# Optimization experiments

Measured on AMD Instinct MI355X. Metric: run time of the kernel, lower is better.

The kernel has to match this reference:

```python
import jax, jax.numpy as jnp
import numpy as np

D_MODEL = 1024
NUM_HEADS = 16
D_HEAD = D_MODEL // NUM_HEADS
POS_VOCAB = 512
ROPE_BASE = 10000.0


def _rope_sin_cos(seq_len, d_head, dtype=jnp.float32):
    inv_freq = 1.0 / (ROPE_BASE ** (jnp.arange(0, d_head, 2, dtype=jnp.float32) / d_head))
    pos = jnp.arange(seq_len, dtype=jnp.float32)
    freqs = pos[:, None] * inv_freq[None, :]            # [S, d_head/2]
    sin = jnp.repeat(jnp.sin(freqs), 2, axis=-1)        # [S, d_head] (repeat_interleave)
    cos = jnp.repeat(jnp.cos(freqs), 2, axis=-1)
    return sin.astype(dtype), cos.astype(dtype)


def _rotate_half(x):
    # interleaved pairs: (x0,x1,x2,x3,...) -> (-x1,x0,-x3,x2,...)
    x1 = x[..., ::2]
    x2 = x[..., 1::2]
    return jnp.stack((-x2, x1), axis=-1).reshape(x.shape)


def setup_inputs() -> dict:
    key = jax.random.key(0)
    ks = jax.random.split(key, 12)
    B, S = 2, 2048
    sc = 1.0 / np.sqrt(D_MODEL)
    inp = {
        "x": jax.random.normal(ks[0], (B, S, D_MODEL), jnp.float32),
        "dist_matrix": jax.random.randint(ks[1], (B, S, S), 0, POS_VOCAB, jnp.int32),
        "Wq": jax.random.normal(ks[2], (D_MODEL, D_MODEL), jnp.float32) * sc,
        "bq": jnp.zeros((D_MODEL,), jnp.float32),
        "Wk": jax.random.normal(ks[3], (D_MODEL, D_MODEL), jnp.float32) * sc,
        "bk": jnp.zeros((D_MODEL,), jnp.float32),
        "Wv": jax.random.normal(ks[4], (D_MODEL, D_MODEL), jnp.float32) * sc,
        "bv": jnp.zeros((D_MODEL,), jnp.float32),
        "Wo": jax.random.normal(ks[5], (D_MODEL, D_MODEL), jnp.float32) * sc,
        "bo": jnp.zeros((D_MODEL,), jnp.float32),
        "bias_table": jax.random.normal(ks[6], (POS_VOCAB, NUM_HEADS), jnp.float32) * 0.02,
    }
    return inp


def reference(x, dist_matrix, Wq, bq, Wk, bk, Wv, bv, Wo, bo, bias_table):
    B, S, _ = x.shape
    H, Dh = NUM_HEADS, D_HEAD

    def proj(W, b):
        return (x @ W + b).reshape(B, S, H, Dh).transpose(0, 2, 1, 3)  # [B,H,S,Dh]

    Q = proj(Wq, bq)
    K = proj(Wk, bk)
    V = proj(Wv, bv)

    sin, cos = _rope_sin_cos(S, Dh, x.dtype)  # [S, Dh]
    Q = Q * cos + _rotate_half(Q) * sin
    K = K * cos + _rotate_half(K) * sin

    scores = jnp.einsum("bhqd,bhkd->bhqk", Q, K) / jnp.sqrt(jnp.asarray(Dh, x.dtype))

    pad_mask = dist_matrix < 0                                 # [B,S,S]
    idx = jnp.clip(dist_matrix, 0, None)
    rel_bias = bias_table[idx]                                 # [B,S,S,H]
    rel_bias = jnp.where(pad_mask[..., None], 0.0, rel_bias)
    scores = scores + rel_bias.transpose(0, 3, 1, 2)           # [B,H,S,S]

    attn = jax.nn.softmax(scores, axis=-1)
    out = jnp.einsum("bhqk,bhkd->bhqd", attn, V)
    out = out.transpose(0, 2, 1, 3).reshape(B, S, H * Dh)
    return out @ Wo + bo
```

## Files before the change

### kernel.cpp

```cpp
#include <hip/hip_runtime.h>
#include <hip/hip_bf16.h>
#include <math.h>

#define B_   2
#define S_   2048
#define H_   16
#define DH_  64
#define DM_  1024
#define M_   (B_*S_)
#define PV_  512
#define LOG2E 1.4426950408889634f

typedef __attribute__((ext_vector_type(8))) short bf16x8;
typedef __attribute__((ext_vector_type(4))) float f32x4;

__device__ __forceinline__ float b2f(unsigned short u) {
  union { unsigned int i; float f; } v; v.i = ((unsigned int)u) << 16; return v.f;
}
__device__ __forceinline__ unsigned short f2b(float f) {
  union { float f; unsigned int i; } v; v.f = f;
  return (unsigned short)((v.i + 0x7fffu + ((v.i >> 16) & 1u)) >> 16);
}
__device__ __forceinline__ f32x4 mfma16(bf16x8 a, bf16x8 b, f32x4 c) {
  return __builtin_amdgcn_mfma_f32_16x16x32_bf16(a, b, c, 0, 0, 0);
}
__device__ __forceinline__ unsigned int cvtpk(float a, float b) {
  unsigned int r;
  asm("v_cvt_pk_bf16_f32 %0, %1, %2" : "=v"(r) : "v"(a), "v"(b));
  return r;
}

__global__ void k_ropetab(float* tab) {
  int idx = blockIdx.x * 256 + threadIdx.x;
  if (idx >= S_ * 32) return;
  int s = idx >> 5, i = idx & 31;
  double inv = exp(-((double)(2 * i) / 64.0) * log(10000.0));
  double f = (double)s * inv;
  tab[idx * 2 + 0] = (float)sin(f);
  tab[idx * 2 + 1] = (float)cos(f);
}

__global__ __launch_bounds__(256) void k_prep(const float* __restrict__ x,
                                              const float* __restrict__ Wq,
                                              const float* __restrict__ Wk,
                                              const float* __restrict__ Wv,
                                              const float* __restrict__ Wo,
                                              float* __restrict__ tab,
                                              unsigned short* __restrict__ Wtall,
                                              unsigned short* __restrict__ xb) {
  __shared__ unsigned short t[64][65];
  int bid = blockIdx.x;
  if (bid < 256) {
    int idx = bid * 256 + threadIdx.x;
    int s = idx >> 5, i = idx & 31;
    double inv = exp(-((double)(2 * i) / 64.0) * log(10000.0));
    double f = (double)s * inv;
    tab[idx * 2 + 0] = (float)sin(f);
    tab[idx * 2 + 1] = (float)cos(f);
  } else if (bid < 1280) {
    int tw = bid - 256;
    int wid = tw >> 8, sub = tw & 255;
    const float* W = (wid == 0) ? Wq : (wid == 1) ? Wk : (wid == 2) ? Wv : Wo;
    unsigned short* Wt = Wtall + (size_t)wid * DM_ * DM_;
    int r0 = (sub >> 4) * 64, c0 = (sub & 15) * 64;
    #pragma unroll
    for (int p = 0; p < 16; ++p) {
      int idx = p * 256 + threadIdx.x;
      int i = idx >> 6, j = idx & 63;
      t[i][j] = f2b(W[(size_t)(r0 + i) * DM_ + c0 + j]);
    }
    __syncthreads();
    #pragma unroll
    for (int p = 0; p < 16; ++p) {
      int idx = p * 256 + threadIdx.x;
      int i = idx >> 6, j = idx & 63;
      Wt[(size_t)(c0 + i) * DM_ + r0 + j] = t[j][i];
    }
  } else {
    int idx = (bid - 1280) * 256 + threadIdx.x;
    const float4 f0 = *(const float4*)(x + (size_t)idx * 8);
    const float4 f1 = *(const float4*)(x + (size_t)idx * 8 + 4);
    union { uint4 u; unsigned short s[8]; } o;
    o.s[0] = f2b(f0.x); o.s[1] = f2b(f0.y); o.s[2] = f2b(f0.z); o.s[3] = f2b(f0.w);
    o.s[4] = f2b(f1.x); o.s[5] = f2b(f1.y); o.s[6] = f2b(f1.z); o.s[7] = f2b(f1.w);
    *(uint4*)(xb + (size_t)idx * 8) = o.u;
  }
}

__global__ __launch_bounds__(256) void k_gemmQKV(const unsigned short* __restrict__ A,
                                                 const unsigned short* __restrict__ Wtall,
                                                 const float* __restrict__ bq,
                                                 const float* __restrict__ bk,
                                                 const float* __restrict__ bv,
                                                 unsigned short* __restrict__ Qr,
                                                 unsigned short* __restrict__ Kr,
                                                 unsigned short* __restrict__ Vp,
                                                 const float* __restrict__ tab,
                                                 float qscale) {
  __shared__ unsigned short Alds[128][40];
  __shared__ unsigned short Blds[128][40];
  int lane = threadIdx.x & 63, w = threadIdx.x >> 6;
  int wr = w >> 1, wc = w & 1;
  int l16 = lane & 15, lq = lane >> 4;
  int m0 = blockIdx.y * 128, n0 = blockIdx.x * 128;
  f32x4 acc[4][4];
  #pragma unroll
  for (int a = 0; a < 4; ++a)
    #pragma unroll
    for (int b = 0; b < 4; ++b) acc[a][b] = (f32x4){0.f, 0.f, 0.f, 0.f};

  for (int k0 = 0; k0 < DM_; k0 += 32) {
    __syncthreads();
    #pragma unroll
    for (int i = 0; i < 2; ++i) {
      int c = threadIdx.x + i * 256;
      int r = c >> 2, ch = (c & 3) * 8;
      *(uint4*)&Alds[r][ch] = *(const uint4*)(A + (size_t)(m0 + r) * DM_ + k0 + ch);
      *(uint4*)&Blds[r][ch] = *(const uint4*)(Wtall + (size_t)(n0 + r) * DM_ + k0 + ch);
    }
    __syncthreads();
    bf16x8 af[4], bf_[4];
    #pragma unroll
    for (int mi = 0; mi < 4; ++mi) af[mi] = *(const bf16x8*)&Alds[wr * 64 + mi * 16 + l16][lq * 8];
    #pragma unroll
    for (int ni = 0; ni < 4; ++ni) bf_[ni] = *(const bf16x8*)&Blds[wc * 64 + ni * 16 + l16][lq * 8];
    #pragma unroll
    for (int mi = 0; mi < 4; ++mi)
      #pragma unroll
      for (int ni = 0; ni < 4; ++ni)
        acc[mi][ni] = mfma16(af[mi], bf_[ni], acc[mi][ni]);
  }

  int proj = n0 >> 10;
  const float* bs = (proj == 0) ? bq : (proj == 1) ? bk : bv;
  float scale = (proj == 0) ? qscale : 1.0f;
  unsigned short* R = (proj == 0) ? Qr : Kr;
  #pragma unroll
  for (int ni = 0; ni < 4; ++ni) {
    int col = n0 + wc * 64 + ni * 16 + l16;
    int c = col & 1023;
    float bvv = bs[c];
    if (proj < 2) {
      int h = c >> 6, d = c & 63;
      #pragma unroll
      for (int mi = 0; mi < 4; ++mi)
        #pragma unroll
        for (int j = 0; j < 4; ++j) {
          int row = m0 + wr * 64 + mi * 16 + lq * 4 + j;
          int s = row & (S_ - 1), b = row >> 11;
          float v = acc[mi][ni][j] + bvv;
          float p = __shfl_xor(v, 1, 64);
          float2 sc = *(const float2*)(tab + ((size_t)s * 32 + (d >> 1)) * 2);
          float o = (d & 1) ? (v * sc.y + p * sc.x)
                            : (v * sc.y - p * sc.x);
          R[(((size_t)(b * H_ + h) * S_) + s) * DH_ + d] = f2b(o * scale);
        }
    } else {
      #pragma unroll
      for (int mi = 0; mi < 4; ++mi)
        #pragma unroll
        for (int j = 0; j < 4; ++j) {
          int row = m0 + wr * 64 + mi * 16 + lq * 4 + j;
          Vp[(size_t)row * DM_ + c] = f2b(acc[mi][ni][j] + bvv);
        }
    }
  }
}

template<bool AF32, bool ROPE, bool OF32, bool WB16>
__global__ __launch_bounds__(256) void k_gemmW(const void* __restrict__ Av,
                                               const void* __restrict__ Wv,
                                               const float* __restrict__ bias,
                                               void* __restrict__ Cv,
                                               const float* __restrict__ tab,
                                               int M, int N, int K, float scale) {
  __shared__ unsigned short Alds[128][40];
  __shared__ unsigned short Blds[128][40];
  int lane = threadIdx.x & 63, w = threadIdx.x >> 6;
  int wr = w >> 1, wc = w & 1;
  int l16 = lane & 15, lq = lane >> 4;
  int m0 = blockIdx.y * 128, n0 = blockIdx.x * 128;
  f32x4 acc[4][4];
  #pragma unroll
  for (int a = 0; a < 4; ++a)
    #pragma unroll
    for (int b = 0; b < 4; ++b) acc[a][b] = (f32x4){0.f, 0.f, 0.f, 0.f};

  for (int k0 = 0; k0 < K; k0 += 32) {
    __syncthreads();
    #pragma unroll
    for (int i = 0; i < 2; ++i) {
      int c = threadIdx.x + i * 256;
      int r = c >> 2, ch = (c & 3) * 8;
      size_t base = (size_t)(m0 + r) * K + k0 + ch;
      if (AF32) {
        const float* A = (const float*)Av;
        float4 f0 = *(const float4*)(A + base);
        float4 f1 = *(const float4*)(A + base + 4);
        unsigned short* dst = &Alds[r][ch];
        dst[0] = f2b(f0.x); dst[1] = f2b(f0.y); dst[2] = f2b(f0.z); dst[3] = f2b(f0.w);
        dst[4] = f2b(f1.x); dst[5] = f2b(f1.y); dst[6] = f2b(f1.z); dst[7] = f2b(f1.w);
      } else {
        *(uint4*)&Alds[r][ch] = *(const uint4*)((const unsigned short*)Av + base);
      }
    }
    if (WB16) {
      #pragma unroll
      for (int i = 0; i < 2; ++i) {
        int c = threadIdx.x + i * 256;
        int r = c >> 2, ch = (c & 3) * 8;
        *(uint4*)&Blds[r][ch] =
            *(const uint4*)((const unsigned short*)Wv + (size_t)(n0 + r) * K + k0 + ch);
      }
    } else {
      #pragma unroll
      for (int i = 0; i < 2; ++i) {
        int c = threadIdx.x + i * 256;
        int kk = c >> 4, n8 = (c & 15) * 8;
        size_t base = (size_t)(k0 + kk) * N + n0 + n8;
        const float* W = (const float*)Wv;
        float4 w0 = *(const float4*)(W + base);
        float4 w1 = *(const float4*)(W + base + 4);
        Blds[n8 + 0][kk] = f2b(w0.x); Blds[n8 + 1][kk] = f2b(w0.y);
        Blds[n8 + 2][kk] = f2b(w0.z); Blds[n8 + 3][kk] = f2b(w0.w);
        Blds[n8 + 4][kk] = f2b(w1.x); Blds[n8 + 5][kk] = f2b(w1.y);
        Blds[n8 + 6][kk] = f2b(w1.z); Blds[n8 + 7][kk] = f2b(w1.w);
      }
    }
    __syncthreads();
    bf16x8 af[4], bf_[4];
    #pragma unroll
    for (int mi = 0; mi < 4; ++mi) af[mi] = *(const bf16x8*)&Alds[wr * 64 + mi * 16 + l16][lq * 8];
    #pragma unroll
    for (int ni = 0; ni < 4; ++ni) bf_[ni] = *(const bf16x8*)&Blds[wc * 64 + ni * 16 + l16][lq * 8];
    #pragma unroll
    for (int mi = 0; mi < 4; ++mi)
      #pragma unroll
      for (int ni = 0; ni < 4; ++ni)
        acc[mi][ni] = mfma16(af[mi], bf_[ni], acc[mi][ni]);
  }
  if (!ROPE) {
    #pragma unroll
    for (int ni = 0; ni < 4; ++ni) {
      int col = n0 + wc * 64 + ni * 16 + l16;
      float bv = bias[col];
      #pragma unroll
      for (int mi = 0; mi < 4; ++mi)
        #pragma unroll
        for (int j = 0; j < 4; ++j) {
          int row = m0 + wr * 64 + mi * 16 + lq * 4 + j;
          size_t idx = (size_t)row * N + col;
          float v = acc[mi][ni][j] + bv;
          if (OF32) ((float*)Cv)[idx] = v;
          else      ((unsigned short*)Cv)[idx] = f2b(v);
        }
    }
  } else {
    #pragma unroll
    for (int ni = 0; ni < 4; ++ni) {
      int col = n0 + wc * 64 + ni * 16 + l16;
      int h = col >> 6, d = col & 63;
      float bv = bias[col];
      #pragma unroll
      for (int mi = 0; mi < 4; ++mi)
        #pragma unroll
        for (int j = 0; j < 4; ++j) {
          int row = m0 + wr * 64 + mi * 16 + lq * 4 + j;
          int s = row & (S_ - 1), b = row >> 11;
          float v = acc[mi][ni][j] + bv;
          float p = __shfl_xor(v, 1, 64);
          float2 sc = *(const float2*)(tab + ((size_t)s * 32 + (d >> 1)) * 2);
          float o = (d & 1) ? (v * sc.y + p * sc.x)
                            : (v * sc.y - p * sc.x);
          ((unsigned short*)Cv)[(((size_t)(b * H_ + h) * S_) + s) * DH_ + d] = f2b(o * scale);
        }
    }
  }
}

__global__ __launch_bounds__(256) void k_vtrans(const unsigned short* __restrict__ Vp,
                                                unsigned short* __restrict__ Vt) {
  int bid = blockIdx.x;
  int st = bid & 31; int bh = bid >> 5; int h = bh & 15; int b = bh >> 4;
  int s0 = st * 64;
  __shared__ unsigned short t[64][72];
  #pragma unroll
  for (int i = 0; i < 2; ++i) {
    int c = threadIdx.x + i * 256;
    int r = c >> 3, ch = (c & 7) * 8;
    *(uint4*)&t[r][ch] = *(const uint4*)(Vp + (size_t)(b * S_ + s0 + r) * DM_ + h * DH_ + ch);
  }
  __syncthreads();
  #pragma unroll
  for (int i = 0; i < 2; ++i) {
    int c = threadIdx.x + i * 256;
    int dr = c >> 3, ch = (c & 7) * 8;
    union { uint4 u; unsigned short x[8]; } tb;
    #pragma unroll
    for (int e = 0; e < 8; ++e) tb.x[e] = t[ch + e][dr];
    *(uint4*)(Vt + ((size_t)bh * DH_ + dr) * S_ + s0 + ch) = tb.u;
  }
}

__global__ __launch_bounds__(512) void k_attn(const unsigned short* __restrict__ Qr,
                                              const unsigned short* __restrict__ Kr,
                                              const unsigned short* __restrict__ Vt,
                                              const int* __restrict__ dist,
                                              const float* __restrict__ table,
                                              unsigned short* __restrict__ AO) {
  int bid = blockIdx.x;
  int qt = bid & 15; int bh = bid >> 4; int h = bh & 15; int b = bh >> 4;
  int lane = threadIdx.x & 63, w = threadIdx.x >> 6;
  int l16 = lane & 15, lq = lane >> 4;
  int q0 = qt * 128;

  __shared__ unsigned short Klds[64][72];
  __shared__ unsigned short Vlds[64][72];
  __shared__ unsigned short Plds[8][16][72];
  __shared__ float tlds[PV_];

  for (int i = threadIdx.x; i < PV_; i += 512) tlds[i] = table[i * H_ + h] * LOG2E;

  const unsigned short* Qbase = Qr + ((size_t)bh * S_ + q0 + w * 16 + l16) * DH_;
  bf16x8 aq0 = *(const bf16x8*)(Qbase + lq * 8);
  bf16x8 aq1 = *(const bf16x8*)(Qbase + 32 + lq * 8);

  f32x4 oacc[4];
  float m_[4], l_[4];
  #pragma unroll
  for (int j = 0; j < 4; ++j) { m_[j] = -1e30f; l_[j] = 0.f; }
  #pragma unroll
  for (int td = 0; td < 4; ++td) oacc[td] = (f32x4){0.f, 0.f, 0.f, 0.f};

  const int* drow = dist + ((size_t)b * S_ + q0 + w * 16) * S_;
  const unsigned short* Ksrc0 = Kr + (size_t)bh * S_ * DH_;
  const unsigned short* Vsrc0 = Vt + (size_t)bh * DH_ * S_;

  int dc[4][4], dn[4][4];
  #pragma unroll
  for (int j = 0; j < 4; ++j) {
    const int* dr = drow + (size_t)(lq * 4 + j) * S_;
    #pragma unroll
    for (int t = 0; t < 4; ++t) dc[j][t] = dr[t * 16 + l16];
  }

  for (int kv = 0; kv < S_; kv += 64) {
    __syncthreads();
    {
      const unsigned short* Ksrc = Ksrc0 + (size_t)kv * DH_;
      const unsigned short* Vsrc = Vsrc0 + kv;
      int c = threadIdx.x;
      int r = c >> 3, ch = (c & 7) * 8;
      *(uint4*)&Klds[r][ch] = *(const uint4*)(Ksrc + (size_t)r * DH_ + ch);
      *(uint4*)&Vlds[r][ch] = *(const uint4*)(Vsrc + (size_t)r * S_ + ch);
    }
    {
      int kvn = (kv + 64 < S_) ? kv + 64 : 0;
      #pragma unroll
      for (int j = 0; j < 4; ++j) {
        const int* dr = drow + (size_t)(lq * 4 + j) * S_ + kvn;
        #pragma unroll
        for (int t = 0; t < 4; ++t) dn[j][t] = dr[t * 16 + l16];
      }
    }
    __syncthreads();

    f32x4 sc[4];
    #pragma unroll
    for (int t = 0; t < 4; ++t) {
      bf16x8 bk0 = *(const bf16x8*)&Klds[t * 16 + l16][lq * 8];
      bf16x8 bk1 = *(const bf16x8*)&Klds[t * 16 + l16][32 + lq * 8];
      f32x4 z = (f32x4){0.f, 0.f, 0.f, 0.f};
      z = mfma16(aq0, bk0, z);
      z = mfma16(aq1, bk1, z);
      sc[t] = z;
    }

    float rm[4];
    #pragma unroll
    for (int j = 0; j < 4; ++j) {
      float best = -1e30f;
      #pragma unroll
      for (int t = 0; t < 4; ++t) {
        float s = sc[t][j] + tlds[dc[j][t]];
        sc[t][j] = s;
        best = fmaxf(best, s);
      }
      rm[j] = best;
    }

    bool need = (rm[0] > m_[0] + 11.5416f) || (rm[1] > m_[1] + 11.5416f) ||
                (rm[2] > m_[2] + 11.5416f) || (rm[3] > m_[3] + 11.5416f);
    if (__any(need)) {
      #pragma unroll
      for (int off = 1; off < 16; off <<= 1) {
        #pragma unroll
        for (int j = 0; j < 4; ++j) rm[j] = fmaxf(rm[j], __shfl_xor(rm[j], off, 64));
      }
      #pragma unroll
      for (int j = 0; j < 4; ++j) {
        float mn = fmaxf(m_[j], rm[j]);
        float scl = exp2f(m_[j] - mn);
        l_[j] *= scl;
        #pragma unroll
        for (int td = 0; td < 4; ++td) oacc[td][j] *= scl;
        m_[j] = mn;
      }
    }

    float p[4][4];
    #pragma unroll
    for (int j = 0; j < 4; ++j) {
      float su = 0.f;
      #pragma unroll
      for (int t = 0; t < 4; ++t) {
        float e = exp2f(sc[t][j] - m_[j]);
        p[t][j] = e;
        su += e;
      }
      l_[j] += su;
    }

    #pragma unroll
    for (int j = 0; j < 4; ++j) {
      unsigned int r01 = cvtpk(p[0][j], p[1][j]);
      unsigned int r23 = cvtpk(p[2][j], p[3][j]);
      Plds[w][lq * 4 + j][l16]      = (unsigned short)r01;
      Plds[w][lq * 4 + j][16 + l16] = (unsigned short)(r01 >> 16);
      Plds[w][lq * 4 + j][32 + l16] = (unsigned short)r23;
      Plds[w][lq * 4 + j][48 + l16] = (unsigned short)(r23 >> 16);
    }

    bf16x8 pa0 = *(const bf16x8*)&Plds[w][l16][lq * 8];
    bf16x8 pa1 = *(const bf16x8*)&Plds[w][l16][32 + lq * 8];
    #pragma unroll
    for (int td = 0; td < 4; ++td) {
      bf16x8 v0 = *(const bf16x8*)&Vlds[td * 16 + l16][lq * 8];
      bf16x8 v1 = *(const bf16x8*)&Vlds[td * 16 + l16][32 + lq * 8];
      oacc[td] = mfma16(pa0, v0, oacc[td]);
      oacc[td] = mfma16(pa1, v1, oacc[td]);
    }

    #pragma unroll
    for (int j = 0; j < 4; ++j)
      #pragma unroll
      for (int t = 0; t < 4; ++t) dc[j][t] = dn[j][t];
  }

  #pragma unroll
  for (int off = 1; off < 16; off <<= 1) {
    #pragma unroll
    for (int j = 0; j < 4; ++j) l_[j] += __shfl_xor(l_[j], off, 64);
  }
  float inv[4];
  #pragma unroll
  for (int j = 0; j < 4; ++j) inv[j] = 1.f / l_[j];
  #pragma unroll
  for (int td = 0; td < 4; ++td) {
    #pragma unroll
    for (int j = 0; j < 4; ++j) {
      size_t row = (size_t)b * S_ + q0 + w * 16 + lq * 4 + j;
      AO[row * DM_ + h * DH_ + td * 16 + l16] = f2b(oacc[td][j] * inv[j]);
    }
  }
}

extern "C" void kernel_launch(void* const* d_in, const int* in_sizes, int n_in,
                              void* d_out, int out_size, void* d_ws, size_t ws_size,
                              hipStream_t stream) {
  const float* x    = (const float*)d_in[0];
  const int*   dist = (const int*)d_in[1];
  const float* Wq   = (const float*)d_in[2];
  const float* bq   = (const float*)d_in[3];
  const float* Wk   = (const float*)d_in[4];
  const float* bk   = (const float*)d_in[5];
  const float* Wv   = (const float*)d_in[6];
  const float* bv   = (const float*)d_in[7];
  const float* Wo   = (const float*)d_in[8];
  const float* bo   = (const float*)d_in[9];
  const float* tabb = (const float*)d_in[10];

  char* ws = (char*)d_ws;
  const size_t SZ_TAB = (size_t)S_ * 32 * 2 * 4;
  const size_t SZ_T   = (size_t)M_ * DM_ * 2;
  const size_t SZ_W   = (size_t)DM_ * DM_ * 2;
  float* rtab = (float*)ws;
  size_t off = SZ_TAB;
  unsigned short* Qr   = (unsigned short*)(ws + off); off += SZ_T;
  unsigned short* Kr   = (unsigned short*)(ws + off); off += SZ_T;
  unsigned short* Vt   = (unsigned short*)(ws + off); off += SZ_T;
  unsigned short* VpAO = (unsigned short*)(ws + off); off += SZ_T;
  unsigned short* Wtall = (unsigned short*)(ws + off); off += 4 * SZ_W;
  size_t off_prep = off;
  unsigned short* xb   = (unsigned short*)(ws + off); off += SZ_T;
  bool prep  = ws_size >= off_prep;
  bool xcast = ws_size >= off;

  const float QSCALE = 0.125f * LOG2E;

  if (prep && xcast) {
    k_prep<<<dim3(3328), 256, 0, stream>>>(x, Wq, Wk, Wv, Wo, rtab, Wtall, xb);
    k_gemmQKV<<<dim3(24, 32), 256, 0, stream>>>(xb, Wtall, bq, bk, bv, Qr, Kr, VpAO, rtab, QSCALE);
  } else {
    k_ropetab<<<dim3(256), dim3(256), 0, stream>>>(rtab);
    k_gemmW<true, true,  false, false><<<dim3(8, 32), 256, 0, stream>>>(x, Wq, bq, Qr, rtab, M_, DM_, DM_, QSCALE);
    k_gemmW<true, true,  false, false><<<dim3(8, 32), 256, 0, stream>>>(x, Wk, bk, Kr, rtab, M_, DM_, DM_, 1.0f);
    k_gemmW<true, false, false, false><<<dim3(8, 32), 256, 0, stream>>>(x, Wv, bv, VpAO, rtab, M_, DM_, DM_, 1.0f);
  }
  k_vtrans<<<dim3(1024), 256, 0, stream>>>(VpAO, Vt);

  k_attn<<<dim3(512), dim3(512), 0, stream>>>(Qr, Kr, Vt, dist, tabb, VpAO);

  if (prep && xcast) {
    k_gemmW<false, false, true, true><<<dim3(8, 32), 256, 0, stream>>>(
        VpAO, Wtall + (size_t)3 * DM_ * DM_, bo, d_out, rtab, M_, DM_, DM_, 1.0f);
  } else {
    k_gemmW<false, false, true, false><<<dim3(8, 32), 256, 0, stream>>>(VpAO, Wo, bo, d_out, rtab, M_, DM_, DM_, 1.0f);
  }
}
```

Baseline: 203.9 us.

## Double-buffer K/V tiles in LDS with register prefetch in attention loop

The attention kernel now keeps two LDS buffers each for K and V. The next K/V tile is loaded from global memory into registers at the start of an iteration and written to the other buffer after the current tile's MFMAs finish. This lets the global load latency overlap with the QK^T, softmax and PV work, and removes one of the two block barriers per iteration. In exchange it doubles the K/V shared memory and keeps extra registers live across the loop, which could lower occupancy.

```diff
diff --git a/kernel.cpp b/kernel.cpp
--- a/kernel.cpp
+++ b/kernel.cpp
@@ -314,8 +314,8 @@
   int l16 = lane & 15, lq = lane >> 4;
   int q0 = qt * 128;
 
-  __shared__ unsigned short Klds[64][72];
-  __shared__ unsigned short Vlds[64][72];
+  __shared__ unsigned short Klds[2][64][72];
+  __shared__ unsigned short Vlds[2][64][72];
   __shared__ unsigned short Plds[8][16][72];
   __shared__ float tlds[PV_];
 
@@ -336,6 +336,8 @@
   const unsigned short* Ksrc0 = Kr + (size_t)bh * S_ * DH_;
   const unsigned short* Vsrc0 = Vt + (size_t)bh * DH_ * S_;
 
+  int sr = threadIdx.x >> 3, sch = (threadIdx.x & 7) * 8;
+
   int dc[4][4], dn[4][4];
   #pragma unroll
   for (int j = 0; j < 4; ++j) {
@@ -344,18 +346,21 @@
     for (int t = 0; t < 4; ++t) dc[j][t] = dr[t * 16 + l16];
   }
 
-  for (int kv = 0; kv < S_; kv += 64) {
+  uint4 krg = *(const uint4*)(Ksrc0 + (size_t)sr * DH_ + sch);
+  uint4 vrg = *(const uint4*)(Vsrc0 + (size_t)sr * S_ + sch);
+  *(uint4*)&Klds[0][sr][sch] = krg;
+  *(uint4*)&Vlds[0][sr][sch] = vrg;
+
+  int cur = 0;
+  for (int kv = 0; kv < S_; kv += 64, cur ^= 1) {
     __syncthreads();
+    bool more = (kv + 64 < S_);
+    if (more) {
+      krg = *(const uint4*)(Ksrc0 + (size_t)(kv + 64 + sr) * DH_ + sch);
+      vrg = *(const uint4*)(Vsrc0 + (size_t)sr * S_ + kv + 64 + sch);
+    }
     {
-      const unsigned short* Ksrc = Ksrc0 + (size_t)kv * DH_;
-      const unsigned short* Vsrc = Vsrc0 + kv;
-      int c = threadIdx.x;
-      int r = c >> 3, ch = (c & 7) * 8;
-      *(uint4*)&Klds[r][ch] = *(const uint4*)(Ksrc + (size_t)r * DH_ + ch);
-      *(uint4*)&Vlds[r][ch] = *(const uint4*)(Vsrc + (size_t)r * S_ + ch);
-    }
-    {
-      int kvn = (kv + 64 < S_) ? kv + 64 : 0;
+      int kvn = more ? kv + 64 : 0;
       #pragma unroll
       for (int j = 0; j < 4; ++j) {
         const int* dr = drow + (size_t)(lq * 4 + j) * S_ + kvn;
@@ -363,13 +368,12 @@
         for (int t = 0; t < 4; ++t) dn[j][t] = dr[t * 16 + l16];
       }
     }
-    __syncthreads();
 
     f32x4 sc[4];
     #pragma unroll
     for (int t = 0; t < 4; ++t) {
-      bf16x8 bk0 = *(const bf16x8*)&Klds[t * 16 + l16][lq * 8];
-      bf16x8 bk1 = *(const bf16x8*)&Klds[t * 16 + l16][32 + lq * 8];
+      bf16x8 bk0 = *(const bf16x8*)&Klds[cur][t * 16 + l16][lq * 8];
+      bf16x8 bk1 = *(const bf16x8*)&Klds[cur][t * 16 + l16][32 + lq * 8];
       f32x4 z = (f32x4){0.f, 0.f, 0.f, 0.f};
       z = mfma16(aq0, bk0, z);
       z = mfma16(aq1, bk1, z);
@@ -435,16 +439,20 @@
     bf16x8 pa1 = *(const bf16x8*)&Plds[w][l16][32 + lq * 8];
     #pragma unroll
     for (int td = 0; td < 4; ++td) {
-      bf16x8 v0 = *(const bf16x8*)&Vlds[td * 16 + l16][lq * 8];
-      bf16x8 v1 = *(const bf16x8*)&Vlds[td * 16 + l16][32 + lq * 8];
+      bf16x8 v0 = *(const bf16x8*)&Vlds[cur][td * 16 + l16][lq * 8];
+      bf16x8 v1 = *(const bf16x8*)&Vlds[cur][td * 16 + l16][32 + lq * 8];
       oacc[td] = mfma16(pa0, v0, oacc[td]);
       oacc[td] = mfma16(pa1, v1, oacc[td]);
     }
 
-    #pragma unroll
-    for (int j = 0; j < 4; ++j)
-      #pragma unroll
-      for (int t = 0; t < 4; ++t) dc[j][t] = dn[j][t];
+    if (more) {
+      *(uint4*)&Klds[cur ^ 1][sr][sch] = krg;
+      *(uint4*)&Vlds[cur ^ 1][sr][sch] = vrg;
+      #pragma unroll
+      for (int j = 0; j < 4; ++j)
+        #pragma unroll
+        for (int t = 0; t < 4; ++t) dc[j][t] = dn[j][t];
+    }
   }
 
   #pragma unroll
```

After: 191.2 us. 1.07x faster.
